# Optimization experiments

Hardware: AMD Instinct MI355X
Metric: run time of the kernel (lower is better)

Reference implementation:

```python
import jax, jax.numpy as jnp
import numpy as np

B, N, D, E = 2, 50000, 128, 640000


def setup_inputs() -> dict:
    key = jax.random.key(0)
    ks = jax.random.split(key, 7)
    x = jax.random.normal(ks[0], (B, N, D), dtype=jnp.float32)
    edge_index = jax.random.randint(ks[1], (2, E), 0, N)
    edge_attr = jax.random.uniform(ks[2], (E,), dtype=jnp.float32)
    s = 1.0 / np.sqrt(D)
    W1 = jax.random.uniform(ks[3], (D, D), jnp.float32, -s, s)
    b1 = jax.random.uniform(ks[4], (D,), jnp.float32, -s, s)
    W2 = jax.random.uniform(ks[5], (D, D), jnp.float32, -s, s)
    b2 = jax.random.uniform(ks[6], (D,), jnp.float32, -s, s)
    return {"x": x, "edge_index": edge_index, "edge_attr": edge_attr,
            "W1": W1, "b1": b1, "W2": W2, "b2": b2}


def _gcn_layer(x, W, b, row, col, norm, n):
    # x: [B, N, D] -> transform then gather-scale-scatter along edges
    h = jnp.einsum('bnd,df->bnf', x, W)
    msg = h[:, row, :] * norm[None, :, None]          # [B, E2, D]
    agg = jax.vmap(lambda m: jax.ops.segment_sum(m, col, num_segments=n))(msg)
    return agg + b


def reference(x, edge_index, edge_attr, W1, b1, W2, b2):
    n = x.shape[1]
    row, col = edge_index[0], edge_index[1]
    # GCNConv default: add self loops (weight 1), symmetric normalization
    loop = jnp.arange(n)
    row2 = jnp.concatenate([row, loop])
    col2 = jnp.concatenate([col, loop])
    w2 = jnp.concatenate([edge_attr, jnp.ones((n,), edge_attr.dtype)])
    deg = jax.ops.segment_sum(w2, col2, num_segments=n)
    dinv = jnp.where(deg > 0, jax.lax.rsqrt(deg), 0.0)
    norm = dinv[row2] * w2 * dinv[col2]               # [E2]
    # dropout is identity in eval mode
    h = jax.nn.relu(_gcn_layer(x, W1, b1, row2, col2, norm, n))
    h = jax.nn.relu(_gcn_layer(h, W2, b2, row2, col2, norm, n))
    return h
```

## Files before the change

### kernel.cpp

```cpp
#include <hip/hip_runtime.h>

#define NNODES 50000
#define NBATCH 2
#define DIM    128
#define NEDGE  640000
#define M_TOT  (NBATCH*NNODES)
#define NXCD   8
#define NBL_N  196

typedef unsigned short u16;
typedef unsigned int   u32;
typedef unsigned long long u64;

typedef __attribute__((ext_vector_type(8))) short bf16x8;
typedef __attribute__((ext_vector_type(4))) float f32x4;

__device__ __forceinline__ float bf2f(u16 u){ return __uint_as_float(((u32)u)<<16); }
__device__ __forceinline__ u16 f2bf(float f){
    u32 x = __float_as_uint(f);
    x += 0x7fffu + ((x>>16)&1u);
    return (u16)(x>>16);
}

__global__ __launch_bounds__(256) void count_k(const int* __restrict__ ei,
                                               const float* __restrict__ ea,
                                               u64* __restrict__ part,
                                               u32* __restrict__ rankpack){
    u32 xcc = __builtin_amdgcn_s_getreg(6164) & 7u;
    int e = blockIdx.x*256 + threadIdx.x;
    if (e < NEDGE){
        int c = ei[NEDGE + e];
        u64 inc = (((u64)__float2uint_rn(ea[e] * 16777216.0f)) << 32) | 1ull;
        u64 old = __hip_atomic_fetch_add(&part[(size_t)xcc*NNODES + c], inc,
                                         __ATOMIC_RELAXED, __HIP_MEMORY_SCOPE_WORKGROUP);
        rankpack[e] = ((u32)old & 0xffffu) | (xcc << 16);
    }
}

__global__ __launch_bounds__(256) void scan1(const u64* __restrict__ part,
                                             int* __restrict__ cnt,
                                             int* __restrict__ poff,
                                             float* __restrict__ dinv,
                                             int* colstart, int* bsum){
    __shared__ int s[256];
    int tid = threadIdx.x;
    int n = blockIdx.x*256 + tid;
    int v = 0;
    if (n < NNODES){
        int run = 0; u64 fsum = 0;
        #pragma unroll
        for (int p = 0; p < NXCD; ++p){
            u64 pv = part[(size_t)p*NNODES + n];
            poff[p*NNODES + n] = run;
            run  += (int)(pv & 0xffffffffu);
            fsum += (pv >> 32);
        }
        cnt[n] = run;
        v = run;
        float deg = 1.0f + (float)fsum * (1.0f/16777216.0f);
        dinv[n] = rsqrtf(deg);
    }
    s[tid] = v; __syncthreads();
    #pragma unroll
    for (int off = 1; off < 256; off <<= 1){
        int t = (tid >= off) ? s[tid-off] : 0;
        __syncthreads();
        s[tid] += t;
        __syncthreads();
    }
    if (n < NNODES) colstart[n] = s[tid] - v;
    if (tid == 255) bsum[blockIdx.x] = s[255];
}

__global__ __launch_bounds__(256) void fill_k(const int* __restrict__ ei,
                                              const float* __restrict__ ea,
                                              const float* __restrict__ dinv,
                                              const int* __restrict__ colstart,
                                              const int* __restrict__ bsum,
                                              const int* __restrict__ poff,
                                              const u32* __restrict__ rankpack,
                                              int* __restrict__ colstartF,
                                              int2* __restrict__ epack){
    __shared__ int s[256];
    __shared__ int pre[256];
    int tid = threadIdx.x;
    int v = (tid < NBL_N) ? bsum[tid] : 0;
    s[tid] = v; __syncthreads();
    #pragma unroll
    for (int off = 1; off < 256; off <<= 1){
        int t = (tid >= off) ? s[tid-off] : 0;
        __syncthreads();
        s[tid] += t;
        __syncthreads();
    }
    pre[tid] = s[tid] - v;
    __syncthreads();

    int e = blockIdx.x*256 + tid;
    if (e < NEDGE){
        int r = ei[e], c = ei[NEDGE + e];
        u32 rp = rankpack[e];
        int base = colstart[c] + pre[c >> 8];
        colstartF[c] = base;
        int pos = base + poff[(rp >> 16)*NNODES + c] + (int)(rp & 0xffffu);
        epack[pos] = make_int2(r, __float_as_int(dinv[r] * ea[e] * dinv[c]));
    }
}

__global__ __launch_bounds__(256) void transposeW(const float* __restrict__ W1, u16* __restrict__ Wt1,
                                                  const float* __restrict__ W2, u16* __restrict__ Wt2){
    int i = blockIdx.x*256 + threadIdx.x;
    const float* W = (i < 16384) ? W1 : W2;
    u16* Wt       = (i < 16384) ? Wt1 : Wt2;
    int ii = i & 16383;
    int k = ii >> 7, n = ii & 127;
    Wt[n*DIM + k] = f2bf(W[ii]);
}

__device__ __forceinline__ bf16x8 load_frag(const float* A, size_t off){
    const float4* ap = (const float4*)(A + off);
    float4 lo = ap[0], hi = ap[1];
    bf16x8 r;
    r[0] = (short)f2bf(lo.x); r[1] = (short)f2bf(lo.y);
    r[2] = (short)f2bf(lo.z); r[3] = (short)f2bf(lo.w);
    r[4] = (short)f2bf(hi.x); r[5] = (short)f2bf(hi.y);
    r[6] = (short)f2bf(hi.z); r[7] = (short)f2bf(hi.w);
    return r;
}
__device__ __forceinline__ bf16x8 load_frag(const u16* A, size_t off){
    return *(const bf16x8*)(A + off);
}

template <typename AT>
__global__ __launch_bounds__(256) void gemm128(const AT* __restrict__ A,
                                               const u16* __restrict__ Wt,
                                               u16* __restrict__ H, int M){
    __shared__ u16 Wl[128][136];
    int tid = threadIdx.x;
    {
        const uint4* src = (const uint4*)Wt;
        #pragma unroll
        for (int j = 0; j < 8; ++j){
            int g = tid + j*256;
            int n = g >> 4;
            int k = (g & 15) * 8;
            *(uint4*)&Wl[n][k] = src[g];
        }
    }
    __syncthreads();

    int wave = tid >> 6, lane = tid & 63;
    int quad = lane >> 4, r = lane & 15;
    int row0 = blockIdx.x*256 + wave*64;

    f32x4 acc[4][8];
    #pragma unroll
    for (int mt = 0; mt < 4; ++mt)
        #pragma unroll
        for (int nt = 0; nt < 8; ++nt)
            acc[mt][nt] = (f32x4){0.f,0.f,0.f,0.f};

    #pragma unroll
    for (int ks = 0; ks < 4; ++ks){
        bf16x8 af[4];
        #pragma unroll
        for (int mt = 0; mt < 4; ++mt){
            int row = row0 + mt*16 + r;
            if (row < M)
                af[mt] = load_frag(A, (size_t)row*DIM + ks*32 + quad*8);
            else
                af[mt] = (bf16x8){0,0,0,0,0,0,0,0};
        }
        #pragma unroll
        for (int nt = 0; nt < 8; ++nt){
            bf16x8 bfr = *(const bf16x8*)&Wl[nt*16 + r][ks*32 + quad*8];
            #pragma unroll
            for (int mt = 0; mt < 4; ++mt)
                acc[mt][nt] = __builtin_amdgcn_mfma_f32_16x16x32_bf16(af[mt], bfr, acc[mt][nt], 0, 0, 0);
        }
    }

    #pragma unroll
    for (int mt = 0; mt < 4; ++mt){
        #pragma unroll
        for (int reg = 0; reg < 4; ++reg){
            int row = row0 + mt*16 + quad*4 + reg;
            if (row < M){
                #pragma unroll
                for (int nt = 0; nt < 8; ++nt)
                    H[(size_t)row*DIM + nt*16 + r] = f2bf(acc[mt][nt][reg]);
            }
        }
    }
}

#define EFMA(W_, V_)                                        \
    a0 = fmaf(W_, bf2f((u16)((V_) & 0xffff)), a0);          \
    a1 = fmaf(W_, bf2f((u16)((V_) >> 16)),    a1);

template <bool OUT_F32>
__global__ __launch_bounds__(256) void gather3_k(const u16* __restrict__ H,
                                                 const int2* __restrict__ epack,
                                                 const int* __restrict__ colstartF,
                                                 const int* __restrict__ cnt,
                                                 const float* __restrict__ dinv,
                                                 const float* __restrict__ bias,
                                                 void* __restrict__ out){
    int wave = threadIdx.x >> 6, lane = threadIdx.x & 63;
    int batch = blockIdx.x & 1;
    int n = (blockIdx.x >> 1)*4 + wave;
    if (n >= NNODES) return;
    const u32* Hb = (const u32*)H + (size_t)batch*NNODES*64;

    int c = __builtin_amdgcn_readfirstlane(cnt[n]);
    int s = (c > 0) ? __builtin_amdgcn_readfirstlane(colstartF[n]) : 0;

    float dn = dinv[n], dn2 = dn*dn;
    u32 sv = Hb[(size_t)n*64 + lane];
    float a0 = dn2*bf2f((u16)(sv & 0xffff));
    float a1 = dn2*bf2f((u16)(sv >> 16));

    const int2* ep = epack + s;
    int j = 0;
    for (; j + 8 <= c; j += 8){
        int2 e0 = ep[j+0], e1 = ep[j+1], e2 = ep[j+2], e3 = ep[j+3];
        int2 e4 = ep[j+4], e5 = ep[j+5], e6 = ep[j+6], e7 = ep[j+7];
        u32 v0 = Hb[(size_t)(u32)e0.x*64 + lane];
        u32 v1 = Hb[(size_t)(u32)e1.x*64 + lane];
        u32 v2 = Hb[(size_t)(u32)e2.x*64 + lane];
        u32 v3 = Hb[(size_t)(u32)e3.x*64 + lane];
        u32 v4 = Hb[(size_t)(u32)e4.x*64 + lane];
        u32 v5 = Hb[(size_t)(u32)e5.x*64 + lane];
        u32 v6 = Hb[(size_t)(u32)e6.x*64 + lane];
        u32 v7 = Hb[(size_t)(u32)e7.x*64 + lane];
        EFMA(__int_as_float(e0.y), v0)
        EFMA(__int_as_float(e1.y), v1)
        EFMA(__int_as_float(e2.y), v2)
        EFMA(__int_as_float(e3.y), v3)
        EFMA(__int_as_float(e4.y), v4)
        EFMA(__int_as_float(e5.y), v5)
        EFMA(__int_as_float(e6.y), v6)
        EFMA(__int_as_float(e7.y), v7)
    }
    for (; j < c; ++j){
        int2 e = ep[j];
        u32 v = Hb[(size_t)(u32)e.x*64 + lane];
        EFMA(__int_as_float(e.y), v)
    }

    float2 bb = ((const float2*)bias)[lane];
    a0 = fmaxf(a0 + bb.x, 0.f);
    a1 = fmaxf(a1 + bb.y, 0.f);
    if (OUT_F32){
        float2* O = (float2*)out;
        O[(size_t)(batch*NNODES + n)*64 + lane] = make_float2(a0, a1);
    } else {
        u32* O = (u32*)out;
        O[(size_t)(batch*NNODES + n)*64 + lane] = (u32)f2bf(a0) | ((u32)f2bf(a1) << 16);
    }
}

extern "C" void kernel_launch(void* const* d_in, const int* in_sizes, int n_in,
                              void* d_out, int out_size, void* d_ws, size_t ws_size,
                              hipStream_t stream){
    const float* x  = (const float*)d_in[0];
    const int*   ei = (const int*)  d_in[1];
    const float* ea = (const float*)d_in[2];
    const float* W1 = (const float*)d_in[3];
    const float* b1 = (const float*)d_in[4];
    const float* W2 = (const float*)d_in[5];
    const float* b2 = (const float*)d_in[6];

    char* p = (char*)d_ws;
    auto alloc = [&](size_t bytes)->char*{ char* r = p; p += (bytes + 511) & ~(size_t)511; return r; };
    u64*   part     = (u64*)  alloc((size_t)NXCD*NNODES*8);
    u32*   rankpack = (u32*)  alloc((size_t)NEDGE*4);
    int*   poff     = (int*)  alloc((size_t)NXCD*NNODES*4);
    float* dinv     = (float*)alloc(NNODES*4);
    int*   cnt      = (int*)  alloc(NNODES*4);
    int*   colstart = (int*)  alloc(NNODES*4);
    int*   colstartF= (int*)  alloc(NNODES*4);
    int*   bsum     = (int*)  alloc(1024);
    int2*  epack    = (int2*) alloc((size_t)NEDGE*8);
    u16*   Wt1      = (u16*)  alloc(DIM*DIM*2);
    u16*   Wt2      = (u16*)  alloc(DIM*DIM*2);
    u16*   h        = (u16*)  alloc((size_t)M_TOT*DIM*2);
    u16*   o1       = (u16*)  alloc((size_t)M_TOT*DIM*2);

    const int NBL_E = (NEDGE  + 255)/256;
    const int NTILE = (M_TOT + 255)/256;
    const int NBL_G = 2*((NNODES + 3)/4);

    hipMemsetAsync(part, 0, (size_t)NXCD*NNODES*8, stream);
    transposeW<<<128, 256, 0, stream>>>(W1, Wt1, W2, Wt2);
    count_k<<<NBL_E, 256, 0, stream>>>(ei, ea, part, rankpack);
    scan1  <<<NBL_N, 256, 0, stream>>>(part, cnt, poff, dinv, colstart, bsum);
    fill_k <<<NBL_E, 256, 0, stream>>>(ei, ea, dinv, colstart, bsum, poff, rankpack, colstartF, epack);

    gemm128<float><<<NTILE, 256, 0, stream>>>(x, Wt1, h, M_TOT);
    gather3_k<false><<<NBL_G, 256, 0, stream>>>(h, epack, colstartF, cnt, dinv, b1, o1);
    gemm128<u16>  <<<NTILE, 256, 0, stream>>>(o1, Wt2, h, M_TOT);
    gather3_k<true> <<<NBL_G, 256, 0, stream>>>(h, epack, colstartF, cnt, dinv, b2, d_out);
}
```

Measured before the change: 304.2 us.

## Pack edge records to 32 bits and double-buffer neighbor gathers via lane shuffles

Edge records shrink from an int2 (row, fp32 weight) to one u32 holding a 16-bit source index and a bf16 normalized weight. This halves edge-list traffic but rounds the edge weight to bf16. The gather kernel now loads up to 64 edge records cooperatively, one per lane, and broadcasts them with shuffles. It also ping-pongs two 8-entry register buffers, so the next batch of feature-row loads is issued while the current batch is accumulated. The aim is to keep more memory loads in flight per wave, at the cost of extra shuffle instructions and more register pressure.

```diff
diff --git a/kernel.cpp b/kernel.cpp
--- a/kernel.cpp
+++ b/kernel.cpp
@@ -80,7 +80,7 @@
                                               const int* __restrict__ poff,
                                               const u32* __restrict__ rankpack,
                                               int* __restrict__ colstartF,
-                                              int2* __restrict__ epack){
+                                              u32* __restrict__ epk){
     __shared__ int s[256];
     __shared__ int pre[256];
     int tid = threadIdx.x;
@@ -103,7 +103,8 @@
         int base = colstart[c] + pre[c >> 8];
         colstartF[c] = base;
         int pos = base + poff[(rp >> 16)*NNODES + c] + (int)(rp & 0xffffu);
-        epack[pos] = make_int2(r, __float_as_int(dinv[r] * ea[e] * dinv[c]));
+        float w = dinv[r] * ea[e] * dinv[c];
+        epk[pos] = (u32)r | ((u32)f2bf(w) << 16);
     }
 }
 
@@ -194,13 +195,23 @@
     }
 }
 
-#define EFMA(W_, V_)                                        \
-    a0 = fmaf(W_, bf2f((u16)((V_) & 0xffff)), a0);          \
-    a1 = fmaf(W_, bf2f((u16)((V_) >> 16)),    a1);
+#define GATHER_ISSUE(MB_, VB_, JB_)                                      \
+    _Pragma("unroll")                                                    \
+    for (int k = 0; k < 8; ++k){                                         \
+        MB_[k] = __shfl(em, (JB_) + k);                                  \
+        VB_[k] = Hb[(size_t)(MB_[k] & 0xffffu)*64 + lane];               \
+    }
+#define GATHER_CONSUME(MB_, VB_)                                         \
+    _Pragma("unroll")                                                    \
+    for (int k = 0; k < 8; ++k){                                         \
+        float w = __uint_as_float(MB_[k] & 0xffff0000u);                 \
+        a0 = fmaf(w, __uint_as_float(VB_[k] << 16), a0);                 \
+        a1 = fmaf(w, __uint_as_float(VB_[k] & 0xffff0000u), a1);         \
+    }
 
 template <bool OUT_F32>
-__global__ __launch_bounds__(256) void gather3_k(const u16* __restrict__ H,
-                                                 const int2* __restrict__ epack,
+__global__ __launch_bounds__(256) void gather4_k(const u16* __restrict__ H,
+                                                 const u32* __restrict__ epk,
                                                  const int* __restrict__ colstartF,
                                                  const int* __restrict__ cnt,
                                                  const float* __restrict__ dinv,
@@ -212,40 +223,31 @@
     if (n >= NNODES) return;
     const u32* Hb = (const u32*)H + (size_t)batch*NNODES*64;
 
-    int c = __builtin_amdgcn_readfirstlane(cnt[n]);
-    int s = (c > 0) ? __builtin_amdgcn_readfirstlane(colstartF[n]) : 0;
-
     float dn = dinv[n], dn2 = dn*dn;
     u32 sv = Hb[(size_t)n*64 + lane];
     float a0 = dn2*bf2f((u16)(sv & 0xffff));
     float a1 = dn2*bf2f((u16)(sv >> 16));
 
-    const int2* ep = epack + s;
-    int j = 0;
-    for (; j + 8 <= c; j += 8){
-        int2 e0 = ep[j+0], e1 = ep[j+1], e2 = ep[j+2], e3 = ep[j+3];
-        int2 e4 = ep[j+4], e5 = ep[j+5], e6 = ep[j+6], e7 = ep[j+7];
-        u32 v0 = Hb[(size_t)(u32)e0.x*64 + lane];
-        u32 v1 = Hb[(size_t)(u32)e1.x*64 + lane];
-        u32 v2 = Hb[(size_t)(u32)e2.x*64 + lane];
-        u32 v3 = Hb[(size_t)(u32)e3.x*64 + lane];
-        u32 v4 = Hb[(size_t)(u32)e4.x*64 + lane];
-        u32 v5 = Hb[(size_t)(u32)e5.x*64 + lane];
-        u32 v6 = Hb[(size_t)(u32)e6.x*64 + lane];
-        u32 v7 = Hb[(size_t)(u32)e7.x*64 + lane];
-        EFMA(__int_as_float(e0.y), v0)
-        EFMA(__int_as_float(e1.y), v1)
-        EFMA(__int_as_float(e2.y), v2)
-        EFMA(__int_as_float(e3.y), v3)
-        EFMA(__int_as_float(e4.y), v4)
-        EFMA(__int_as_float(e5.y), v5)
-        EFMA(__int_as_float(e6.y), v6)
-        EFMA(__int_as_float(e7.y), v7)
-    }
-    for (; j < c; ++j){
-        int2 e = ep[j];
-        u32 v = Hb[(size_t)(u32)e.x*64 + lane];
-        EFMA(__int_as_float(e.y), v)
+    int s = colstartF[n], c = cnt[n];
+    for (int base = 0; base < c; base += 64){
+        int m = min(64, c - base);
+        u32 em = 0;
+        if (lane < m) em = epk[s + base + lane];
+
+        u32 mA[8], vA[8], mB[8], vB[8];
+        GATHER_ISSUE(mA, vA, 0)
+        bool useA = true;
+        for (int j = 0; j < m; j += 8){
+            int jn = j + 8;
+            if (useA){
+                if (jn < m){ GATHER_ISSUE(mB, vB, jn) }
+                GATHER_CONSUME(mA, vA)
+            } else {
+                if (jn < m){ GATHER_ISSUE(mA, vA, jn) }
+                GATHER_CONSUME(mB, vB)
+            }
+            useA = !useA;
+        }
     }
 
     float2 bb = ((const float2*)bias)[lane];
@@ -281,7 +283,7 @@
     int*   colstart = (int*)  alloc(NNODES*4);
     int*   colstartF= (int*)  alloc(NNODES*4);
     int*   bsum     = (int*)  alloc(1024);
-    int2*  epack    = (int2*) alloc((size_t)NEDGE*8);
+    u32*   epk      = (u32*)  alloc((size_t)NEDGE*4);
     u16*   Wt1      = (u16*)  alloc(DIM*DIM*2);
     u16*   Wt2      = (u16*)  alloc(DIM*DIM*2);
     u16*   h        = (u16*)  alloc((size_t)M_TOT*DIM*2);
@@ -295,10 +297,10 @@
     transposeW<<<128, 256, 0, stream>>>(W1, Wt1, W2, Wt2);
     count_k<<<NBL_E, 256, 0, stream>>>(ei, ea, part, rankpack);
     scan1  <<<NBL_N, 256, 0, stream>>>(part, cnt, poff, dinv, colstart, bsum);
-    fill_k <<<NBL_E, 256, 0, stream>>>(ei, ea, dinv, colstart, bsum, poff, rankpack, colstartF, epack);
+    fill_k <<<NBL_E, 256, 0, stream>>>(ei, ea, dinv, colstart, bsum, poff, rankpack, colstartF, epk);
 
     gemm128<float><<<NTILE, 256, 0, stream>>>(x, Wt1, h, M_TOT);
-    gather3_k<false><<<NBL_G, 256, 0, stream>>>(h, epack, colstartF, cnt, dinv, b1, o1);
+    gather4_k<false><<<NBL_G, 256, 0, stream>>>(h, epk, colstartF, cnt, dinv, b1, o1);
     gemm128<u16>  <<<NTILE, 256, 0, stream>>>(o1, Wt2, h, M_TOT);
-    gather3_k<true> <<<NBL_G, 256, 0, stream>>>(h, epack, colstartF, cnt, dinv, b2, d_out);
-}
+    gather4_k<true> <<<NBL_G, 256, 0, stream>>>(h, epk, colstartF, cnt, dinv, b2, d_out);
+}
```

Measured after the change: 296.7 us. 2.5% less time.
